# Kernel optimization log

Hardware: AMD Instinct MI355X
Metric: run time of the kernel (lower is better)

The kernel has to match this reference:

```python
import jax, jax.numpy as jnp
import numpy as np

L, D, F, H, E, V = 16, 256, 512, 8, 12, 52000  # layers, width, FFWidth, heads, experts, vocab
B, S = 4, 512
HD = D // H
EPS = 1e-5


def _ln(x, s, b):
    m = x.mean(-1, keepdims=True)
    v = ((x - m) ** 2).mean(-1, keepdims=True)
    return (x - m) / jnp.sqrt(v + EPS) * s + b


def setup_inputs() -> dict:
    key = jax.random.key(0)
    ks = jax.random.split(key, 12)
    w = lambda k, shape: (jax.random.normal(k, shape, dtype=jnp.float32) * 0.02)
    return {
        "tokens": jax.random.randint(ks[0], (B, S), 0, V),
        "emb": w(ks[1], (V, D)),
        "Wq": w(ks[2], (L, D, D)), "bq": jnp.zeros((L, D), jnp.float32),
        "Wk": w(ks[3], (L, D, D)), "bk": jnp.zeros((L, D), jnp.float32),
        "Wv": w(ks[4], (L, D, D)), "bv": jnp.zeros((L, D), jnp.float32),
        "ln1_s": jnp.ones((L, D), jnp.float32), "ln1_b": jnp.zeros((L, D), jnp.float32),
        "ln2_s": jnp.ones((L, D), jnp.float32), "ln2_b": jnp.zeros((L, D), jnp.float32),
        "gW": w(ks[5], (L, D, E)), "gb": jnp.zeros((L, E), jnp.float32),
        "ff1W": w(ks[6], (L, E, D, F)), "ff1b": jnp.zeros((L, E, F), jnp.float32),
        "ffGW": w(ks[7], (L, E, D, F)), "ffGb": jnp.zeros((L, E, F), jnp.float32),
        "ff2W": w(ks[8], (L, E, F, D)), "ff2b": jnp.zeros((L, E, D), jnp.float32),
    }


def _forward(tokens, emb, Wq, bq, Wk, bk, Wv, bv, ln1_s, ln1_b, ln2_s, ln2_b,
             gW, gb, ff1W, ff1b, ffGW, ffGb, ff2W, ff2b):
    x = emb[tokens]  # [B,S,D]
    causal = jnp.triu(jnp.full((S, S), -jnp.inf, dtype=x.dtype), 1)

    def body(x, p):
        (wq, bq_, wk, bk_, wv, bv_, l1s, l1b, l2s, l2b,
         gw, gb_, f1w, f1b, fgw, fgb, f2w, f2b) = p
        q = (x @ wq + bq_).reshape(B, S, H, HD)
        k = (x @ wk + bk_).reshape(B, S, H, HD)
        v = (x @ wv + bv_).reshape(B, S, H, HD)
        # NOTE: original applies no 1/sqrt(d) scaling -- kept faithful
        att = jnp.einsum('bshw,bShw->bhsS', q, k) + causal
        att = jax.nn.softmax(att, axis=-1)
        o = jnp.einsum('bhsS,bShw->bshw', att, v).reshape(B, S, D)
        norm = _ln(o + x, l1s, l1b)
        # MoE: top-2 experts, outputs SUMMED (no gate weighting, per original)
        probs = jax.nn.softmax(norm @ gw + gb_, axis=-1)
        _, idx = jax.lax.top_k(probs, 2)  # [B,S,2]
        msk = jax.nn.one_hot(idx, E, dtype=norm.dtype).sum(-2)  # [B,S,E] in {0,1}
        h = jax.nn.silu(jnp.einsum('bsd,edf->bsef', norm, f1w) + f1b) \
            * (jnp.einsum('bsd,edf->bsef', norm, fgw) + fgb)
        y = jnp.einsum('bsef,efd->bsed', h, f2w) + f2b
        moe = jnp.einsum('bsed,bse->bsd', y, msk)
        return _ln(moe + norm, l2s, l2b), None

    x, _ = jax.lax.scan(body, x, (Wq, bq, Wk, bk, Wv, bv, ln1_s, ln1_b, ln2_s, ln2_b,
                                  gW, gb, ff1W, ff1b, ffGW, ffGb, ff2W, ff2b))
    return x


def reference(tokens, emb, Wq, bq, Wk, bk, Wv, bv, ln1_s, ln1_b, ln2_s, ln2_b,
              gW, gb, ff1W, ff1b, ffGW, ffGb, ff2W, ff2b):
    return _forward(tokens, emb, Wq, bq, Wk, bk, Wv, bv, ln1_s, ln1_b, ln2_s, ln2_b,
                    gW, gb, ff1W, ff1b, ffGW, ffGb, ff2W, ff2b)
```

## Files before the change

kernel.cpp:

```cpp
#include <hip/hip_runtime.h>
#include <math.h>

#define LNUM 16
#define D 256
#define FF 512
#define NH 8
#define NE 12
#define HD 32
#define BB 4
#define SS 512
#define NT 2048
#define EPS 1e-5f
#define MAXT 48
#define PADROWS 5632

typedef _Float16 f16;
typedef __attribute__((ext_vector_type(8))) _Float16 f16x8;
typedef __attribute__((ext_vector_type(4))) _Float16 f16x4;
typedef __attribute__((ext_vector_type(4))) float f32x4;
#define MFMA(A, B, C) __builtin_amdgcn_mfma_f32_16x16x32_f16((A), (B), (C), 0, 0, 0)

__device__ inline void splitf(float x, f16& h, f16& l) {
  f16 hh = (f16)x;
  h = hh;
  l = (f16)(x - (float)hh);
}

__global__ __launch_bounds__(256) void k_wprep(const float* __restrict__ src,
                                               f16* __restrict__ dh, f16* __restrict__ dl,
                                               int K, int N) {
  const size_t msz = (size_t)K * N * blockIdx.z;
  src += msz; dh += msz; dl += msz;
  const int n0 = blockIdx.x * 32, k0 = blockIdx.y * 32;
  __shared__ f16 th[32][36], tl[32][36];
  const int t = threadIdx.x;
  {
    const int r = t >> 3, c4 = (t & 7) * 4;
    float4 v = *(const float4*)(src + (size_t)(k0 + r) * N + n0 + c4);
    f16 h0, l0, h1, l1, h2, l2, h3, l3;
    splitf(v.x, h0, l0); splitf(v.y, h1, l1);
    splitf(v.z, h2, l2); splitf(v.w, h3, l3);
    th[c4 + 0][r] = h0; tl[c4 + 0][r] = l0;
    th[c4 + 1][r] = h1; tl[c4 + 1][r] = l1;
    th[c4 + 2][r] = h2; tl[c4 + 2][r] = l2;
    th[c4 + 3][r] = h3; tl[c4 + 3][r] = l3;
  }
  __syncthreads();
  const int rn = t >> 3, ck = (t & 7) * 4;
  f16x4 hv, lv;
#pragma unroll
  for (int j = 0; j < 4; j++) { hv[j] = th[rn][ck + j]; lv[j] = tl[rn][ck + j]; }
  *(f16x4*)(dh + (size_t)(n0 + rn) * K + k0 + ck) = hv;
  *(f16x4*)(dl + (size_t)(n0 + rn) * K + k0 + ck) = lv;
}

__global__ __launch_bounds__(256) void k_embed(const int* __restrict__ tok,
                                               const float* __restrict__ emb,
                                               float* __restrict__ x,
                                               f16* __restrict__ xh, f16* __restrict__ xl) {
  int n = blockIdx.x, t = threadIdx.x;
  float val = emb[(size_t)tok[n] * D + t];
  x[(size_t)n * D + t] = val;
  f16 h, l; splitf(val, h, l);
  xh[(size_t)n * D + t] = h;
  xl[(size_t)n * D + t] = l;
}

__global__ __launch_bounds__(256) void k_qkv_mfma(
    const f16* __restrict__ xh, const f16* __restrict__ xl,
    const f16* __restrict__ wqh, const f16* __restrict__ wql, const float* __restrict__ bq,
    const f16* __restrict__ wkh, const f16* __restrict__ wkl, const float* __restrict__ bk,
    const f16* __restrict__ wvh, const f16* __restrict__ wvl, const float* __restrict__ bv,
    f16* __restrict__ qhb, f16* __restrict__ qlb,
    f16* __restrict__ khb, f16* __restrict__ klb,
    f16* __restrict__ vhb, f16* __restrict__ vlb) {
  const f16* Wh; const f16* Wl; const float* bias; f16* outh; f16* outl;
  if (blockIdx.z == 0)      { Wh = wqh; Wl = wql; bias = bq; outh = qhb; outl = qlb; }
  else if (blockIdx.z == 1) { Wh = wkh; Wl = wkl; bias = bk; outh = khb; outl = klb; }
  else                      { Wh = wvh; Wl = wvl; bias = bv; outh = vhb; outl = vlb; }
  const int row0 = blockIdx.x * 128, col0 = blockIdx.y * 64;
  __shared__ f16 Ah[128][44], Al[128][44], Bh[64][44], Bl[64][44];
  const int tid = threadIdx.x;
  const int asr = tid >> 1, asc = (tid & 1) * 16;
  const int bn2 = tid >> 2, bkc = (tid & 3) * 8;
  const int lane = tid & 63, w = tid >> 6;
  const int lm = lane & 15, lg = lane >> 4, lk = lg * 8;
  f32x4 acc[2][4] = {};
  for (int k0 = 0; k0 < D; k0 += 32) {
    {
      size_t ga = (size_t)(row0 + asr) * D + k0 + asc;
      *(f16x8*)&Ah[asr][asc]     = *(const f16x8*)(xh + ga);
      *(f16x8*)&Ah[asr][asc + 8] = *(const f16x8*)(xh + ga + 8);
      *(f16x8*)&Al[asr][asc]     = *(const f16x8*)(xl + ga);
      *(f16x8*)&Al[asr][asc + 8] = *(const f16x8*)(xl + ga + 8);
      size_t gb = (size_t)(col0 + bn2) * D + k0 + bkc;
      *(f16x8*)&Bh[bn2][bkc] = *(const f16x8*)(Wh + gb);
      *(f16x8*)&Bl[bn2][bkc] = *(const f16x8*)(Wl + gb);
    }
    __syncthreads();
    f16x8 a_h[2], a_l[2];
#pragma unroll
    for (int mt = 0; mt < 2; mt++) {
      a_h[mt] = *(const f16x8*)&Ah[w * 32 + mt * 16 + lm][lk];
      a_l[mt] = *(const f16x8*)&Al[w * 32 + mt * 16 + lm][lk];
    }
#pragma unroll
    for (int nt = 0; nt < 4; nt++) {
      f16x8 b_h = *(const f16x8*)&Bh[nt * 16 + lm][lk];
      f16x8 b_l = *(const f16x8*)&Bl[nt * 16 + lm][lk];
#pragma unroll
      for (int mt = 0; mt < 2; mt++) {
        f32x4 c = acc[mt][nt];
        c = MFMA(a_h[mt], b_h, c);
        c = MFMA(a_h[mt], b_l, c);
        c = MFMA(a_l[mt], b_h, c);
        acc[mt][nt] = c;
      }
    }
    __syncthreads();
  }
#pragma unroll
  for (int mt = 0; mt < 2; mt++)
#pragma unroll
    for (int nt = 0; nt < 4; nt++) {
      int col = col0 + nt * 16 + lm;
      float bv_ = bias[col];
#pragma unroll
      for (int r = 0; r < 4; r++) {
        int row = row0 + w * 32 + mt * 16 + lg * 4 + r;
        float val = acc[mt][nt][r] + bv_;
        f16 h16, l16; splitf(val, h16, l16);
        outh[(size_t)row * D + col] = h16;
        outl[(size_t)row * D + col] = l16;
      }
    }
}

__global__ __launch_bounds__(256) void k_attn_mfma(
    const f16* __restrict__ qh, const f16* __restrict__ ql,
    const f16* __restrict__ kh, const f16* __restrict__ kl,
    const f16* __restrict__ vh, const f16* __restrict__ vl,
    float* __restrict__ o) {
  const int rt = blockIdx.x, bh = blockIdx.y;
  const int b = bh >> 3, h = bh & 7;
  const int row0 = rt * 64;
  __shared__ f16 Qh[64][40], Ql[64][40], Kh[64][40], Kl[64][40];
  __shared__ f16 Vth[32][72], Vtl[32][72];
  __shared__ f16 Ph[4][16][72], Pl[4][16][72];
  const int tid = threadIdx.x;
  const int lane = tid & 63, w = tid >> 6;
  const int lm = lane & 15, lg = lane >> 4, lk = lg * 8;
  const int sr = tid >> 2, sc = (tid & 3) * 8;
  {
    size_t gq = (size_t)(b * SS + row0 + sr) * D + h * HD + sc;
    *(f16x8*)&Qh[sr][sc] = *(const f16x8*)(qh + gq);
    *(f16x8*)&Ql[sr][sc] = *(const f16x8*)(ql + gq);
  }
  f32x4 accO[2] = {};
  float mrow[4], lsum[4];
#pragma unroll
  for (int r = 0; r < 4; r++) { mrow[r] = -1e30f; lsum[r] = 0.f; }
  for (int ct = 0; ct <= rt; ct++) {
    __syncthreads();
    {
      size_t gk = (size_t)(b * SS + ct * 64 + sr) * D + h * HD + sc;
      *(f16x8*)&Kh[sr][sc] = *(const f16x8*)(kh + gk);
      *(f16x8*)&Kl[sr][sc] = *(const f16x8*)(kl + gk);
      f16x8 hv = *(const f16x8*)(vh + gk);
      f16x8 lv = *(const f16x8*)(vl + gk);
#pragma unroll
      for (int j = 0; j < 8; j++) { Vth[sc + j][sr] = hv[j]; Vtl[sc + j][sr] = lv[j]; }
    }
    __syncthreads();
    f16x8 qfh = *(const f16x8*)&Qh[w * 16 + lm][lk];
    f16x8 qfl = *(const f16x8*)&Ql[w * 16 + lm][lk];
    f32x4 s[4];
#pragma unroll
    for (int nt = 0; nt < 4; nt++) {
      f16x8 kfh = *(const f16x8*)&Kh[nt * 16 + lm][lk];
      f16x8 kfl = *(const f16x8*)&Kl[nt * 16 + lm][lk];
      f32x4 c = {};
      c = MFMA(qfh, kfh, c);
      c = MFMA(qfh, kfl, c);
      c = MFMA(qfl, kfh, c);
      s[nt] = c;
    }
    if (ct == rt) {
#pragma unroll
      for (int nt = 0; nt < 4; nt++)
#pragma unroll
        for (int r = 0; r < 4; r++)
          if (nt * 16 + lm > w * 16 + lg * 4 + r) s[nt][r] = -1e30f;
    }
    float scal[4];
#pragma unroll
    for (int r = 0; r < 4; r++) {
      float mt2 = fmaxf(fmaxf(s[0][r], s[1][r]), fmaxf(s[2][r], s[3][r]));
      mt2 = fmaxf(mt2, __shfl_xor(mt2, 1));
      mt2 = fmaxf(mt2, __shfl_xor(mt2, 2));
      mt2 = fmaxf(mt2, __shfl_xor(mt2, 4));
      mt2 = fmaxf(mt2, __shfl_xor(mt2, 8));
      float mn = fmaxf(mrow[r], mt2);
      scal[r] = expf(mrow[r] - mn);
      mrow[r] = mn;
    }
    float rs[4] = {0.f, 0.f, 0.f, 0.f};
#pragma unroll
    for (int nt = 0; nt < 4; nt++)
#pragma unroll
      for (int r = 0; r < 4; r++) {
        float pv = expf(s[nt][r] - mrow[r]);
        rs[r] += pv;
        f16 ph16, pl16; splitf(pv, ph16, pl16);
        Ph[w][lg * 4 + r][nt * 16 + lm] = ph16;
        Pl[w][lg * 4 + r][nt * 16 + lm] = pl16;
      }
#pragma unroll
    for (int r = 0; r < 4; r++) {
      rs[r] += __shfl_xor(rs[r], 1);
      rs[r] += __shfl_xor(rs[r], 2);
      rs[r] += __shfl_xor(rs[r], 4);
      rs[r] += __shfl_xor(rs[r], 8);
      lsum[r] = lsum[r] * scal[r] + rs[r];
      accO[0][r] *= scal[r];
      accO[1][r] *= scal[r];
    }
#pragma unroll
    for (int ct2 = 0; ct2 < 2; ct2++)
#pragma unroll
      for (int ks = 0; ks < 2; ks++) {
        f16x8 pa_h = *(const f16x8*)&Ph[w][lm][ks * 32 + lk];
        f16x8 pa_l = *(const f16x8*)&Pl[w][lm][ks * 32 + lk];
        f16x8 vb_h = *(const f16x8*)&Vth[ct2 * 16 + lm][ks * 32 + lk];
        f16x8 vb_l = *(const f16x8*)&Vtl[ct2 * 16 + lm][ks * 32 + lk];
        accO[ct2] = MFMA(pa_h, vb_h, accO[ct2]);
        accO[ct2] = MFMA(pa_h, vb_l, accO[ct2]);
        accO[ct2] = MFMA(pa_l, vb_h, accO[ct2]);
      }
  }
#pragma unroll
  for (int ct2 = 0; ct2 < 2; ct2++)
#pragma unroll
    for (int r = 0; r < 4; r++) {
      int grow = row0 + w * 16 + lg * 4 + r;
      o[(size_t)(b * SS + grow) * D + h * HD + ct2 * 16 + lm] = accO[ct2][r] / lsum[r];
    }
}

__global__ __launch_bounds__(256) void k_ln1gate(
    const float* __restrict__ o, const float* __restrict__ x,
    const float* __restrict__ s1, const float* __restrict__ b1,
    const float* __restrict__ gW, const float* __restrict__ gb,
    float* __restrict__ norm, f16* __restrict__ nhb, f16* __restrict__ nlb,
    int* __restrict__ eidx) {
  const int w = threadIdx.x >> 6, lane = threadIdx.x & 63;
  const int n = blockIdx.x * 4 + w;
  float val[4], s1v = 0.f, s2v = 0.f;
#pragma unroll
  for (int j = 0; j < 4; j++) {
    int d = lane + 64 * j;
    float v = o[(size_t)n * D + d] + x[(size_t)n * D + d];
    val[j] = v; s1v += v; s2v += v * v;
  }
#pragma unroll
  for (int m = 1; m < 64; m <<= 1) {
    s1v += __shfl_xor(s1v, m);
    s2v += __shfl_xor(s2v, m);
  }
  float mean = s1v * (1.f / D);
  float var = s2v * (1.f / D) - mean * mean;
  float rstd = rsqrtf(var + EPS);
  float ge[NE];
#pragma unroll
  for (int e = 0; e < NE; e++) ge[e] = 0.f;
#pragma unroll
  for (int j = 0; j < 4; j++) {
    int d = lane + 64 * j;
    float nv = (val[j] - mean) * rstd * s1[d] + b1[d];
    norm[(size_t)n * D + d] = nv;
    f16 h16, l16; splitf(nv, h16, l16);
    nhb[(size_t)n * D + d] = h16;
    nlb[(size_t)n * D + d] = l16;
    const float* gr = gW + (size_t)d * NE;
#pragma unroll
    for (int e = 0; e < NE; e++) ge[e] += nv * gr[e];
  }
#pragma unroll
  for (int m = 1; m < 64; m <<= 1)
#pragma unroll
    for (int e = 0; e < NE; e++) ge[e] += __shfl_xor(ge[e], m);
  if (lane == 0) {
#pragma unroll
    for (int e = 0; e < NE; e++) ge[e] += gb[e];
    int i1 = 0; float v1 = ge[0];
#pragma unroll
    for (int e = 1; e < NE; e++) if (ge[e] > v1) { v1 = ge[e]; i1 = e; }
    int i2 = -1; float v2 = -3.4e38f;
#pragma unroll
    for (int e = 0; e < NE; e++) if (e != i1 && ge[e] > v2) { v2 = ge[e]; i2 = e; }
    eidx[n * 2 + 0] = i1;
    eidx[n * 2 + 1] = i2;
  }
}

__global__ __launch_bounds__(256) void k_route(const int* __restrict__ eidx,
                                               int* __restrict__ rlist, int* __restrict__ tokpos,
                                               int* __restrict__ te, int* __restrict__ tbase,
                                               int* __restrict__ tnv) {
  __shared__ int cnt[NE], cur[NE], poff[NE];
  const int t = threadIdx.x;
  if (t < NE) { cnt[t] = 0; cur[t] = 0; }
  __syncthreads();
  for (int n = t; n < NT; n += 256) {
    atomicAdd(&cnt[eidx[n * 2 + 0]], 1);
    atomicAdd(&cnt[eidx[n * 2 + 1]], 1);
  }
  __syncthreads();
  if (t == 0) {
    int off = 0, ti = 0;
    for (int e = 0; e < NE; e++) {
      poff[e] = off;
      int ntl = (cnt[e] + 127) >> 7;
      for (int tt = 0; tt < ntl; tt++) {
        te[ti] = e; tbase[ti] = off + tt * 128;
        int rem = cnt[e] - tt * 128; tnv[ti] = rem < 128 ? rem : 128;
        ti++;
      }
      off += ntl * 128;
    }
    for (; ti < MAXT; ti++) te[ti] = -1;
  }
  __syncthreads();
  for (int n = t; n < NT; n += 256) {
#pragma unroll
    for (int s2 = 0; s2 < 2; s2++) {
      int e = eidx[n * 2 + s2];
      int pos = atomicAdd(&cur[e], 1);
      int row = poff[e] + pos;
      rlist[row] = n;
      tokpos[n * 2 + s2] = row;
    }
  }
}

__global__ __launch_bounds__(256) void k_ff1_mfma(
    const f16* __restrict__ nhb, const f16* __restrict__ nlb,
    const int* __restrict__ rlist,
    const int* __restrict__ te, const int* __restrict__ tbase, const int* __restrict__ tnv,
    const f16* __restrict__ w1th, const f16* __restrict__ w1tl, const float* __restrict__ b1f,
    const f16* __restrict__ wgth, const f16* __restrict__ wgtl, const float* __restrict__ bgf,
    f16* __restrict__ hhb, f16* __restrict__ hlb) {
  const int mt0 = blockIdx.x;
  const int e = te[mt0];
  if (e < 0) return;
  const int base = tbase[mt0], nv = tnv[mt0];
  const int col0 = blockIdx.y * 64;
  const f16* W1h = w1th + (size_t)e * D * FF;
  const f16* W1l = w1tl + (size_t)e * D * FF;
  const f16* Wgh = wgth + (size_t)e * D * FF;
  const f16* Wgl = wgtl + (size_t)e * D * FF;
  __shared__ f16 Ah[128][44], Al[128][44];
  __shared__ f16 B1h[64][44], B1l[64][44], B2h[64][44], B2l[64][44];
  __shared__ int rows[128];
  const int tid = threadIdx.x;
  if (tid < 128) rows[tid] = (tid < nv) ? rlist[base + tid] : 0;
  __syncthreads();
  const int asr = tid >> 1, asc = (tid & 1) * 16;
  const int bn2 = tid >> 2, bkc = (tid & 3) * 8;
  const int lane = tid & 63, w = tid >> 6;
  const int lm = lane & 15, lg = lane >> 4, lk = lg * 8;
  f32x4 acc1[2][4] = {}, acc2[2][4] = {};
  const int arow = rows[asr];
  for (int k0 = 0; k0 < D; k0 += 32) {
    {
      size_t ga = (size_t)arow * D + k0 + asc;
      *(f16x8*)&Ah[asr][asc]     = *(const f16x8*)(nhb + ga);
      *(f16x8*)&Ah[asr][asc + 8] = *(const f16x8*)(nhb + ga + 8);
      *(f16x8*)&Al[asr][asc]     = *(const f16x8*)(nlb + ga);
      *(f16x8*)&Al[asr][asc + 8] = *(const f16x8*)(nlb + ga + 8);
      size_t gb = (size_t)(col0 + bn2) * D + k0 + bkc;
      *(f16x8*)&B1h[bn2][bkc] = *(const f16x8*)(W1h + gb);
      *(f16x8*)&B1l[bn2][bkc] = *(const f16x8*)(W1l + gb);
      *(f16x8*)&B2h[bn2][bkc] = *(const f16x8*)(Wgh + gb);
      *(f16x8*)&B2l[bn2][bkc] = *(const f16x8*)(Wgl + gb);
    }
    __syncthreads();
    f16x8 a_h[2], a_l[2];
#pragma unroll
    for (int mt = 0; mt < 2; mt++) {
      a_h[mt] = *(const f16x8*)&Ah[w * 32 + mt * 16 + lm][lk];
      a_l[mt] = *(const f16x8*)&Al[w * 32 + mt * 16 + lm][lk];
    }
#pragma unroll
    for (int nt = 0; nt < 4; nt++) {
      f16x8 b_h = *(const f16x8*)&B1h[nt * 16 + lm][lk];
      f16x8 b_l = *(const f16x8*)&B1l[nt * 16 + lm][lk];
      f16x8 c_h = *(const f16x8*)&B2h[nt * 16 + lm][lk];
      f16x8 c_l = *(const f16x8*)&B2l[nt * 16 + lm][lk];
#pragma unroll
      for (int mt = 0; mt < 2; mt++) {
        f32x4 c1 = acc1[mt][nt];
        c1 = MFMA(a_h[mt], b_h, c1);
        c1 = MFMA(a_h[mt], b_l, c1);
        c1 = MFMA(a_l[mt], b_h, c1);
        acc1[mt][nt] = c1;
        f32x4 c2 = acc2[mt][nt];
        c2 = MFMA(a_h[mt], c_h, c2);
        c2 = MFMA(a_h[mt], c_l, c2);
        c2 = MFMA(a_l[mt], c_h, c2);
        acc2[mt][nt] = c2;
      }
    }
    __syncthreads();
  }
#pragma unroll
  for (int mt = 0; mt < 2; mt++)
#pragma unroll
    for (int nt = 0; nt < 4; nt++) {
      int col = col0 + nt * 16 + lm;
      float bb1 = b1f[e * FF + col], bb2 = bgf[e * FF + col];
#pragma unroll
      for (int r = 0; r < 4; r++) {
        int rit = w * 32 + mt * 16 + lg * 4 + r;
        if (rit < nv) {
          float z1 = acc1[mt][nt][r] + bb1;
          float zg = acc2[mt][nt][r] + bb2;
          float sl = z1 / (1.f + expf(-z1));
          float hv = sl * zg;
          f16 h16, l16; splitf(hv, h16, l16);
          hhb[(size_t)(base + rit) * FF + col] = h16;
          hlb[(size_t)(base + rit) * FF + col] = l16;
        }
      }
    }
}

__global__ __launch_bounds__(256) void k_ff2_mfma(
    const f16* __restrict__ hhb, const f16* __restrict__ hlb,
    const int* __restrict__ te, const int* __restrict__ tbase, const int* __restrict__ tnv,
    const f16* __restrict__ w2th, const f16* __restrict__ w2tl, const float* __restrict__ b2f,
    float* __restrict__ ybuf) {
  const int mt0 = blockIdx.x;
  const int e = te[mt0];
  if (e < 0) return;
  const int base = tbase[mt0], nv = tnv[mt0];
  const int col0 = blockIdx.y * 64;
  const f16* W2h = w2th + (size_t)e * FF * D;
  const f16* W2l = w2tl + (size_t)e * FF * D;
  __shared__ f16 Ah[128][44], Al[128][44], Bh[64][44], Bl[64][44];
  const int tid = threadIdx.x;
  const int asr = tid >> 1, asc = (tid & 1) * 16;
  const int bn2 = tid >> 2, bkc = (tid & 3) * 8;
  const int lane = tid & 63, w = tid >> 6;
  const int lm = lane & 15, lg = lane >> 4, lk = lg * 8;
  f32x4 acc[2][4] = {};
  for (int k0 = 0; k0 < FF; k0 += 32) {
    {
      size_t ga = (size_t)(base + asr) * FF + k0 + asc;
      *(f16x8*)&Ah[asr][asc]     = *(const f16x8*)(hhb + ga);
      *(f16x8*)&Ah[asr][asc + 8] = *(const f16x8*)(hhb + ga + 8);
      *(f16x8*)&Al[asr][asc]     = *(const f16x8*)(hlb + ga);
      *(f16x8*)&Al[asr][asc + 8] = *(const f16x8*)(hlb + ga + 8);
      size_t gb = (size_t)(col0 + bn2) * FF + k0 + bkc;
      *(f16x8*)&Bh[bn2][bkc] = *(const f16x8*)(W2h + gb);
      *(f16x8*)&Bl[bn2][bkc] = *(const f16x8*)(W2l + gb);
    }
    __syncthreads();
    f16x8 a_h[2], a_l[2];
#pragma unroll
    for (int mt = 0; mt < 2; mt++) {
      a_h[mt] = *(const f16x8*)&Ah[w * 32 + mt * 16 + lm][lk];
      a_l[mt] = *(const f16x8*)&Al[w * 32 + mt * 16 + lm][lk];
    }
#pragma unroll
    for (int nt = 0; nt < 4; nt++) {
      f16x8 b_h = *(const f16x8*)&Bh[nt * 16 + lm][lk];
      f16x8 b_l = *(const f16x8*)&Bl[nt * 16 + lm][lk];
#pragma unroll
      for (int mt = 0; mt < 2; mt++) {
        f32x4 c = acc[mt][nt];
        c = MFMA(a_h[mt], b_h, c);
        c = MFMA(a_h[mt], b_l, c);
        c = MFMA(a_l[mt], b_h, c);
        acc[mt][nt] = c;
      }
    }
    __syncthreads();
  }
#pragma unroll
  for (int mt = 0; mt < 2; mt++)
#pragma unroll
    for (int nt = 0; nt < 4; nt++) {
      int col = col0 + nt * 16 + lm;
      float bb = b2f[e * D + col];
#pragma unroll
      for (int r = 0; r < 4; r++) {
        int rit = w * 32 + mt * 16 + lg * 4 + r;
        if (rit < nv) ybuf[(size_t)(base + rit) * D + col] = acc[mt][nt][r] + bb;
      }
    }
}

__global__ __launch_bounds__(256) void k_ln2(
    const float* __restrict__ ybuf, const int* __restrict__ tokpos,
    const float* __restrict__ norm, const float* __restrict__ s2, const float* __restrict__ b2,
    float* __restrict__ dst, f16* __restrict__ xh, f16* __restrict__ xl) {
  const int w = threadIdx.x >> 6, lane = threadIdx.x & 63;
  const int n = blockIdx.x * 4 + w;
  const int p0 = tokpos[n * 2 + 0], p1 = tokpos[n * 2 + 1];
  float val[4], s1v = 0.f, s2v = 0.f;
#pragma unroll
  for (int j = 0; j < 4; j++) {
    int d = lane + 64 * j;
    float v = ybuf[(size_t)p0 * D + d] + ybuf[(size_t)p1 * D + d] + norm[(size_t)n * D + d];
    val[j] = v; s1v += v; s2v += v * v;
  }
#pragma unroll
  for (int m = 1; m < 64; m <<= 1) {
    s1v += __shfl_xor(s1v, m);
    s2v += __shfl_xor(s2v, m);
  }
  float mean = s1v * (1.f / D);
  float var = s2v * (1.f / D) - mean * mean;
  float rstd = rsqrtf(var + EPS);
#pragma unroll
  for (int j = 0; j < 4; j++) {
    int d = lane + 64 * j;
    float ov = (val[j] - mean) * rstd * s2[d] + b2[d];
    dst[(size_t)n * D + d] = ov;
    f16 h16, l16; splitf(ov, h16, l16);
    xh[(size_t)n * D + d] = h16;
    xl[(size_t)n * D + d] = l16;
  }
}

extern "C" void kernel_launch(void* const* d_in, const int* in_sizes, int n_in,
                              void* d_out, int out_size, void* d_ws, size_t ws_size,
                              hipStream_t stream) {
  (void)in_sizes; (void)n_in; (void)out_size; (void)ws_size;
  const int*   tok = (const int*)d_in[0];
  const float* emb = (const float*)d_in[1];
  const float* Wq  = (const float*)d_in[2];
  const float* bq  = (const float*)d_in[3];
  const float* Wk  = (const float*)d_in[4];
  const float* bk  = (const float*)d_in[5];
  const float* Wv  = (const float*)d_in[6];
  const float* bv  = (const float*)d_in[7];
  const float* l1s = (const float*)d_in[8];
  const float* l1b = (const float*)d_in[9];
  const float* l2s = (const float*)d_in[10];
  const float* l2b = (const float*)d_in[11];
  const float* gW  = (const float*)d_in[12];
  const float* gb  = (const float*)d_in[13];
  const float* f1W = (const float*)d_in[14];
  const float* f1b = (const float*)d_in[15];
  const float* fgW = (const float*)d_in[16];
  const float* fgb = (const float*)d_in[17];
  const float* f2W = (const float*)d_in[18];
  const float* f2b = (const float*)d_in[19];
  float* out = (float*)d_out;

  char* p = (char*)d_ws;
  auto alloc = [&](size_t bytes) { char* r = p; p += (bytes + 255) & ~(size_t)255; return r; };
  float* xb = (float*)alloc((size_t)NT * D * 4);
  f16* xh = (f16*)alloc((size_t)NT * D * 2);
  f16* xl = (f16*)alloc((size_t)NT * D * 2);
  f16* qhb = (f16*)alloc((size_t)NT * D * 2);
  f16* qlb = (f16*)alloc((size_t)NT * D * 2);
  f16* khb = (f16*)alloc((size_t)NT * D * 2);
  f16* klb = (f16*)alloc((size_t)NT * D * 2);
  f16* vhb = (f16*)alloc((size_t)NT * D * 2);
  f16* vlb = (f16*)alloc((size_t)NT * D * 2);
  float* ob = (float*)alloc((size_t)NT * D * 4);
  float* nb = (float*)alloc((size_t)NT * D * 4);
  f16* nhb = (f16*)alloc((size_t)NT * D * 2);
  f16* nlb = (f16*)alloc((size_t)NT * D * 2);
  f16* hhb = (f16*)alloc((size_t)PADROWS * FF * 2);
  f16* hlb = (f16*)alloc((size_t)PADROWS * FF * 2);
  float* yb = (float*)alloc((size_t)PADROWS * D * 4);
  int* eidx   = (int*)alloc((size_t)NT * 2 * 4);
  int* rlist  = (int*)alloc((size_t)PADROWS * 4);
  int* tokpos = (int*)alloc((size_t)NT * 2 * 4);
  int* te     = (int*)alloc(MAXT * 4);
  int* tbase  = (int*)alloc(MAXT * 4);
  int* tnv    = (int*)alloc(MAXT * 4);
  size_t qkvsz = (size_t)LNUM * D * D;
  size_t ffsz  = (size_t)LNUM * NE * D * FF;
  f16* wqh = (f16*)alloc(qkvsz * 2); f16* wql = (f16*)alloc(qkvsz * 2);
  f16* wkh = (f16*)alloc(qkvsz * 2); f16* wkl = (f16*)alloc(qkvsz * 2);
  f16* wvh = (f16*)alloc(qkvsz * 2); f16* wvl = (f16*)alloc(qkvsz * 2);
  f16* w1th = (f16*)alloc(ffsz * 2); f16* w1tl = (f16*)alloc(ffsz * 2);
  f16* wgth = (f16*)alloc(ffsz * 2); f16* wgtl = (f16*)alloc(ffsz * 2);
  f16* w2th = (f16*)alloc(ffsz * 2); f16* w2tl = (f16*)alloc(ffsz * 2);

  k_wprep<<<dim3(D / 32, D / 32, LNUM), 256, 0, stream>>>(Wq, wqh, wql, D, D);
  k_wprep<<<dim3(D / 32, D / 32, LNUM), 256, 0, stream>>>(Wk, wkh, wkl, D, D);
  k_wprep<<<dim3(D / 32, D / 32, LNUM), 256, 0, stream>>>(Wv, wvh, wvl, D, D);
  k_wprep<<<dim3(FF / 32, D / 32, LNUM * NE), 256, 0, stream>>>(f1W, w1th, w1tl, D, FF);
  k_wprep<<<dim3(FF / 32, D / 32, LNUM * NE), 256, 0, stream>>>(fgW, wgth, wgtl, D, FF);
  k_wprep<<<dim3(D / 32, FF / 32, LNUM * NE), 256, 0, stream>>>(f2W, w2th, w2tl, FF, D);

  k_embed<<<NT, 256, 0, stream>>>(tok, emb, xb, xh, xl);

  for (int l = 0; l < LNUM; l++) {
    k_qkv_mfma<<<dim3(16, 4, 3), 256, 0, stream>>>(
        xh, xl,
        wqh + (size_t)l * D * D, wql + (size_t)l * D * D, bq + (size_t)l * D,
        wkh + (size_t)l * D * D, wkl + (size_t)l * D * D, bk + (size_t)l * D,
        wvh + (size_t)l * D * D, wvl + (size_t)l * D * D, bv + (size_t)l * D,
        qhb, qlb, khb, klb, vhb, vlb);
    k_attn_mfma<<<dim3(8, 32), 256, 0, stream>>>(qhb, qlb, khb, klb, vhb, vlb, ob);
    k_ln1gate<<<NT / 4, 256, 0, stream>>>(ob, xb, l1s + (size_t)l * D, l1b + (size_t)l * D,
                                          gW + (size_t)l * D * NE, gb + (size_t)l * NE,
                                          nb, nhb, nlb, eidx);
    k_route<<<1, 256, 0, stream>>>(eidx, rlist, tokpos, te, tbase, tnv);
    k_ff1_mfma<<<dim3(MAXT, 8), 256, 0, stream>>>(
        nhb, nlb, rlist, te, tbase, tnv,
        w1th + (size_t)l * NE * D * FF, w1tl + (size_t)l * NE * D * FF, f1b + (size_t)l * NE * FF,
        wgth + (size_t)l * NE * D * FF, wgtl + (size_t)l * NE * D * FF, fgb + (size_t)l * NE * FF,
        hhb, hlb);
    k_ff2_mfma<<<dim3(MAXT, 4), 256, 0, stream>>>(
        hhb, hlb, te, tbase, tnv,
        w2th + (size_t)l * NE * FF * D, w2tl + (size_t)l * NE * FF * D, f2b + (size_t)l * NE * D,
        yb);
    k_ln2<<<NT / 4, 256, 0, stream>>>(yb, tokpos, nb, l2s + (size_t)l * D, l2b + (size_t)l * D,
                                      (l == LNUM - 1) ? out : xb, xh, xl);
  }
}
```

Before: 1.974 ms.

## Fold MoE routing into gate kernel with fixed-capacity expert slots; widen K tiles

Drops the single-block k_route kernel. The gate kernel now claims per-expert row slots with atomics into fixed-capacity regions (CAP rows per expert), and the FF kernels derive their tiles from per-layer counters that are zeroed once in the embed kernel. The GEMM kernels also move from a K-step of 32 to 64 with larger padded LDS tiles, halving the number of barrier rounds. The attention MFMA sections are wrapped in s_setprio. The cost removed is the serial per-layer routing launch and its latency. The trade-off is that an expert receiving more than 512 tokens would overflow its slot region, and atomic slot order makes row placement nondeterministic.

After: 2.254 ms. +14.2%, slower.

```diff
diff --git a/kernel.cpp b/kernel.cpp
--- a/kernel.cpp
+++ b/kernel.cpp
@@ -11,8 +11,8 @@
 #define SS 512
 #define NT 2048
 #define EPS 1e-5f
-#define MAXT 48
-#define PADROWS 5632
+#define CAP 512
+#define ROWSP (NE * CAP)
 
 typedef _Float16 f16;
 typedef __attribute__((ext_vector_type(8))) _Float16 f16x8;
@@ -57,8 +57,10 @@
 __global__ __launch_bounds__(256) void k_embed(const int* __restrict__ tok,
                                                const float* __restrict__ emb,
                                                float* __restrict__ x,
-                                               f16* __restrict__ xh, f16* __restrict__ xl) {
+                                               f16* __restrict__ xh, f16* __restrict__ xl,
+                                               int* __restrict__ cntbuf) {
   int n = blockIdx.x, t = threadIdx.x;
+  if (n == 0 && t < LNUM * NE) cntbuf[t] = 0;
   float val = emb[(size_t)tok[n] * D + t];
   x[(size_t)n * D + t] = val;
   f16 h, l; splitf(val, h, l);
@@ -74,47 +76,55 @@
     f16* __restrict__ qhb, f16* __restrict__ qlb,
     f16* __restrict__ khb, f16* __restrict__ klb,
     f16* __restrict__ vhb, f16* __restrict__ vlb) {
+  const int mat = blockIdx.z;
   const f16* Wh; const f16* Wl; const float* bias; f16* outh; f16* outl;
-  if (blockIdx.z == 0)      { Wh = wqh; Wl = wql; bias = bq; outh = qhb; outl = qlb; }
-  else if (blockIdx.z == 1) { Wh = wkh; Wl = wkl; bias = bk; outh = khb; outl = klb; }
-  else                      { Wh = wvh; Wl = wvl; bias = bv; outh = vhb; outl = vlb; }
+  if (mat == 0)      { Wh = wqh; Wl = wql; bias = bq; outh = qhb; outl = qlb; }
+  else if (mat == 1) { Wh = wkh; Wl = wkl; bias = bk; outh = khb; outl = klb; }
+  else               { Wh = wvh; Wl = wvl; bias = bv; outh = vhb; outl = vlb; }
   const int row0 = blockIdx.x * 128, col0 = blockIdx.y * 64;
-  __shared__ f16 Ah[128][44], Al[128][44], Bh[64][44], Bl[64][44];
+  __shared__ f16 Ah[128][72], Al[128][72], Bh[64][72], Bl[64][72];
   const int tid = threadIdx.x;
-  const int asr = tid >> 1, asc = (tid & 1) * 16;
-  const int bn2 = tid >> 2, bkc = (tid & 3) * 8;
+  const int asr = tid >> 1, asc = (tid & 1) * 32;
+  const int bn2 = tid >> 2, bkc = (tid & 3) * 16;
   const int lane = tid & 63, w = tid >> 6;
   const int lm = lane & 15, lg = lane >> 4, lk = lg * 8;
   f32x4 acc[2][4] = {};
-  for (int k0 = 0; k0 < D; k0 += 32) {
+  for (int k0 = 0; k0 < D; k0 += 64) {
     {
       size_t ga = (size_t)(row0 + asr) * D + k0 + asc;
-      *(f16x8*)&Ah[asr][asc]     = *(const f16x8*)(xh + ga);
-      *(f16x8*)&Ah[asr][asc + 8] = *(const f16x8*)(xh + ga + 8);
-      *(f16x8*)&Al[asr][asc]     = *(const f16x8*)(xl + ga);
-      *(f16x8*)&Al[asr][asc + 8] = *(const f16x8*)(xl + ga + 8);
+#pragma unroll
+      for (int j = 0; j < 4; j++) {
+        *(f16x8*)&Ah[asr][asc + j * 8] = *(const f16x8*)(xh + ga + j * 8);
+        *(f16x8*)&Al[asr][asc + j * 8] = *(const f16x8*)(xl + ga + j * 8);
+      }
       size_t gb = (size_t)(col0 + bn2) * D + k0 + bkc;
-      *(f16x8*)&Bh[bn2][bkc] = *(const f16x8*)(Wh + gb);
-      *(f16x8*)&Bl[bn2][bkc] = *(const f16x8*)(Wl + gb);
-    }
-    __syncthreads();
-    f16x8 a_h[2], a_l[2];
-#pragma unroll
-    for (int mt = 0; mt < 2; mt++) {
-      a_h[mt] = *(const f16x8*)&Ah[w * 32 + mt * 16 + lm][lk];
-      a_l[mt] = *(const f16x8*)&Al[w * 32 + mt * 16 + lm][lk];
-    }
-#pragma unroll
-    for (int nt = 0; nt < 4; nt++) {
-      f16x8 b_h = *(const f16x8*)&Bh[nt * 16 + lm][lk];
-      f16x8 b_l = *(const f16x8*)&Bl[nt * 16 + lm][lk];
+#pragma unroll
+      for (int j = 0; j < 2; j++) {
+        *(f16x8*)&Bh[bn2][bkc + j * 8] = *(const f16x8*)(Wh + gb + j * 8);
+        *(f16x8*)&Bl[bn2][bkc + j * 8] = *(const f16x8*)(Wl + gb + j * 8);
+      }
+    }
+    __syncthreads();
+#pragma unroll
+    for (int ks = 0; ks < 2; ks++) {
+      f16x8 a_h[2], a_l[2];
 #pragma unroll
       for (int mt = 0; mt < 2; mt++) {
-        f32x4 c = acc[mt][nt];
-        c = MFMA(a_h[mt], b_h, c);
-        c = MFMA(a_h[mt], b_l, c);
-        c = MFMA(a_l[mt], b_h, c);
-        acc[mt][nt] = c;
+        a_h[mt] = *(const f16x8*)&Ah[w * 32 + mt * 16 + lm][ks * 32 + lk];
+        a_l[mt] = *(const f16x8*)&Al[w * 32 + mt * 16 + lm][ks * 32 + lk];
+      }
+#pragma unroll
+      for (int nt = 0; nt < 4; nt++) {
+        f16x8 b_h = *(const f16x8*)&Bh[nt * 16 + lm][ks * 32 + lk];
+        f16x8 b_l = *(const f16x8*)&Bl[nt * 16 + lm][ks * 32 + lk];
+#pragma unroll
+        for (int mt = 0; mt < 2; mt++) {
+          f32x4 c = acc[mt][nt];
+          c = MFMA(a_h[mt], b_h, c);
+          c = MFMA(a_h[mt], b_l, c);
+          c = MFMA(a_l[mt], b_h, c);
+          acc[mt][nt] = c;
+        }
       }
     }
     __syncthreads();
@@ -175,6 +185,7 @@
     f16x8 qfh = *(const f16x8*)&Qh[w * 16 + lm][lk];
     f16x8 qfl = *(const f16x8*)&Ql[w * 16 + lm][lk];
     f32x4 s[4];
+    __builtin_amdgcn_s_setprio(1);
 #pragma unroll
     for (int nt = 0; nt < 4; nt++) {
       f16x8 kfh = *(const f16x8*)&Kh[nt * 16 + lm][lk];
@@ -185,6 +196,7 @@
       c = MFMA(qfl, kfh, c);
       s[nt] = c;
     }
+    __builtin_amdgcn_s_setprio(0);
     if (ct == rt) {
 #pragma unroll
       for (int nt = 0; nt < 4; nt++)
@@ -225,6 +237,7 @@
       accO[0][r] *= scal[r];
       accO[1][r] *= scal[r];
     }
+    __builtin_amdgcn_s_setprio(1);
 #pragma unroll
     for (int ct2 = 0; ct2 < 2; ct2++)
 #pragma unroll
@@ -237,6 +250,7 @@
         accO[ct2] = MFMA(pa_h, vb_l, accO[ct2]);
         accO[ct2] = MFMA(pa_l, vb_h, accO[ct2]);
       }
+    __builtin_amdgcn_s_setprio(0);
   }
 #pragma unroll
   for (int ct2 = 0; ct2 < 2; ct2++)
@@ -252,7 +266,7 @@
     const float* __restrict__ s1, const float* __restrict__ b1,
     const float* __restrict__ gW, const float* __restrict__ gb,
     float* __restrict__ norm, f16* __restrict__ nhb, f16* __restrict__ nlb,
-    int* __restrict__ eidx) {
+    int* __restrict__ cnt, int* __restrict__ rlist, int* __restrict__ tokpos) {
   const int w = threadIdx.x >> 6, lane = threadIdx.x & 63;
   const int n = blockIdx.x * 4 + w;
   float val[4], s1v = 0.f, s2v = 0.f;
@@ -298,117 +312,91 @@
     int i2 = -1; float v2 = -3.4e38f;
 #pragma unroll
     for (int e = 0; e < NE; e++) if (e != i1 && ge[e] > v2) { v2 = ge[e]; i2 = e; }
-    eidx[n * 2 + 0] = i1;
-    eidx[n * 2 + 1] = i2;
-  }
-}
-
-__global__ __launch_bounds__(256) void k_route(const int* __restrict__ eidx,
-                                               int* __restrict__ rlist, int* __restrict__ tokpos,
-                                               int* __restrict__ te, int* __restrict__ tbase,
-                                               int* __restrict__ tnv) {
-  __shared__ int cnt[NE], cur[NE], poff[NE];
-  const int t = threadIdx.x;
-  if (t < NE) { cnt[t] = 0; cur[t] = 0; }
-  __syncthreads();
-  for (int n = t; n < NT; n += 256) {
-    atomicAdd(&cnt[eidx[n * 2 + 0]], 1);
-    atomicAdd(&cnt[eidx[n * 2 + 1]], 1);
-  }
-  __syncthreads();
-  if (t == 0) {
-    int off = 0, ti = 0;
-    for (int e = 0; e < NE; e++) {
-      poff[e] = off;
-      int ntl = (cnt[e] + 127) >> 7;
-      for (int tt = 0; tt < ntl; tt++) {
-        te[ti] = e; tbase[ti] = off + tt * 128;
-        int rem = cnt[e] - tt * 128; tnv[ti] = rem < 128 ? rem : 128;
-        ti++;
-      }
-      off += ntl * 128;
-    }
-    for (; ti < MAXT; ti++) te[ti] = -1;
-  }
-  __syncthreads();
-  for (int n = t; n < NT; n += 256) {
-#pragma unroll
-    for (int s2 = 0; s2 < 2; s2++) {
-      int e = eidx[n * 2 + s2];
-      int pos = atomicAdd(&cur[e], 1);
-      int row = poff[e] + pos;
-      rlist[row] = n;
-      tokpos[n * 2 + s2] = row;
-    }
+    int p1 = atomicAdd(&cnt[i1], 1);
+    int row1 = i1 * CAP + p1;
+    rlist[row1] = n;
+    tokpos[n * 2 + 0] = row1;
+    int p2 = atomicAdd(&cnt[i2], 1);
+    int row2 = i2 * CAP + p2;
+    rlist[row2] = n;
+    tokpos[n * 2 + 1] = row2;
   }
 }
 
 __global__ __launch_bounds__(256) void k_ff1_mfma(
     const f16* __restrict__ nhb, const f16* __restrict__ nlb,
-    const int* __restrict__ rlist,
-    const int* __restrict__ te, const int* __restrict__ tbase, const int* __restrict__ tnv,
+    const int* __restrict__ cnt, const int* __restrict__ rlist,
     const f16* __restrict__ w1th, const f16* __restrict__ w1tl, const float* __restrict__ b1f,
     const f16* __restrict__ wgth, const f16* __restrict__ wgtl, const float* __restrict__ bgf,
     f16* __restrict__ hhb, f16* __restrict__ hlb) {
-  const int mt0 = blockIdx.x;
-  const int e = te[mt0];
-  if (e < 0) return;
-  const int base = tbase[mt0], nv = tnv[mt0];
+  const int e = blockIdx.x >> 2, tl = blockIdx.x & 3;
+  const int cnt_e = cnt[e];
+  if (tl * 128 >= cnt_e) return;
+  const int nv0 = cnt_e - tl * 128;
+  const int nv = nv0 < 128 ? nv0 : 128;
+  const int base = e * CAP + tl * 128;
   const int col0 = blockIdx.y * 64;
-  const f16* W1h = w1th + (size_t)e * D * FF;
-  const f16* W1l = w1tl + (size_t)e * D * FF;
-  const f16* Wgh = wgth + (size_t)e * D * FF;
-  const f16* Wgl = wgtl + (size_t)e * D * FF;
-  __shared__ f16 Ah[128][44], Al[128][44];
-  __shared__ f16 B1h[64][44], B1l[64][44], B2h[64][44], B2l[64][44];
+  const f16* W1h = w1th + (size_t)e * D * FF + (size_t)col0 * D;
+  const f16* W1l = w1tl + (size_t)e * D * FF + (size_t)col0 * D;
+  const f16* Wgh = wgth + (size_t)e * D * FF + (size_t)col0 * D;
+  const f16* Wgl = wgtl + (size_t)e * D * FF + (size_t)col0 * D;
+  __shared__ f16 Ah[128][72], Al[128][72];
+  __shared__ f16 B1h[64][72], B1l[64][72], B2h[64][72], B2l[64][72];
   __shared__ int rows[128];
   const int tid = threadIdx.x;
   if (tid < 128) rows[tid] = (tid < nv) ? rlist[base + tid] : 0;
   __syncthreads();
-  const int asr = tid >> 1, asc = (tid & 1) * 16;
-  const int bn2 = tid >> 2, bkc = (tid & 3) * 8;
+  const int asr = tid >> 1, asc = (tid & 1) * 32;
+  const int bn2 = tid >> 2, bkc = (tid & 3) * 16;
   const int lane = tid & 63, w = tid >> 6;
   const int lm = lane & 15, lg = lane >> 4, lk = lg * 8;
   f32x4 acc1[2][4] = {}, acc2[2][4] = {};
   const int arow = rows[asr];
-  for (int k0 = 0; k0 < D; k0 += 32) {
+  for (int k0 = 0; k0 < D; k0 += 64) {
     {
       size_t ga = (size_t)arow * D + k0 + asc;
-      *(f16x8*)&Ah[asr][asc]     = *(const f16x8*)(nhb + ga);
-      *(f16x8*)&Ah[asr][asc + 8] = *(const f16x8*)(nhb + ga + 8);
-      *(f16x8*)&Al[asr][asc]     = *(const f16x8*)(nlb + ga);
-      *(f16x8*)&Al[asr][asc + 8] = *(const f16x8*)(nlb + ga + 8);
-      size_t gb = (size_t)(col0 + bn2) * D + k0 + bkc;
-      *(f16x8*)&B1h[bn2][bkc] = *(const f16x8*)(W1h + gb);
-      *(f16x8*)&B1l[bn2][bkc] = *(const f16x8*)(W1l + gb);
-      *(f16x8*)&B2h[bn2][bkc] = *(const f16x8*)(Wgh + gb);
-      *(f16x8*)&B2l[bn2][bkc] = *(const f16x8*)(Wgl + gb);
-    }
-    __syncthreads();
-    f16x8 a_h[2], a_l[2];
-#pragma unroll
-    for (int mt = 0; mt < 2; mt++) {
-      a_h[mt] = *(const f16x8*)&Ah[w * 32 + mt * 16 + lm][lk];
-      a_l[mt] = *(const f16x8*)&Al[w * 32 + mt * 16 + lm][lk];
-    }
-#pragma unroll
-    for (int nt = 0; nt < 4; nt++) {
-      f16x8 b_h = *(const f16x8*)&B1h[nt * 16 + lm][lk];
-      f16x8 b_l = *(const f16x8*)&B1l[nt * 16 + lm][lk];
-      f16x8 c_h = *(const f16x8*)&B2h[nt * 16 + lm][lk];
-      f16x8 c_l = *(const f16x8*)&B2l[nt * 16 + lm][lk];
+#pragma unroll
+      for (int j = 0; j < 4; j++) {
+        *(f16x8*)&Ah[asr][asc + j * 8] = *(const f16x8*)(nhb + ga + j * 8);
+        *(f16x8*)&Al[asr][asc + j * 8] = *(const f16x8*)(nlb + ga + j * 8);
+      }
+      size_t gb = (size_t)bn2 * D + k0 + bkc;
+#pragma unroll
+      for (int j = 0; j < 2; j++) {
+        *(f16x8*)&B1h[bn2][bkc + j * 8] = *(const f16x8*)(W1h + gb + j * 8);
+        *(f16x8*)&B1l[bn2][bkc + j * 8] = *(const f16x8*)(W1l + gb + j * 8);
+        *(f16x8*)&B2h[bn2][bkc + j * 8] = *(const f16x8*)(Wgh + gb + j * 8);
+        *(f16x8*)&B2l[bn2][bkc + j * 8] = *(const f16x8*)(Wgl + gb + j * 8);
+      }
+    }
+    __syncthreads();
+#pragma unroll
+    for (int ks = 0; ks < 2; ks++) {
+      f16x8 a_h[2], a_l[2];
 #pragma unroll
       for (int mt = 0; mt < 2; mt++) {
-        f32x4 c1 = acc1[mt][nt];
-        c1 = MFMA(a_h[mt], b_h, c1);
-        c1 = MFMA(a_h[mt], b_l, c1);
-        c1 = MFMA(a_l[mt], b_h, c1);
-        acc1[mt][nt] = c1;
-        f32x4 c2 = acc2[mt][nt];
-        c2 = MFMA(a_h[mt], c_h, c2);
-        c2 = MFMA(a_h[mt], c_l, c2);
-        c2 = MFMA(a_l[mt], c_h, c2);
-        acc2[mt][nt] = c2;
+        a_h[mt] = *(const f16x8*)&Ah[w * 32 + mt * 16 + lm][ks * 32 + lk];
+        a_l[mt] = *(const f16x8*)&Al[w * 32 + mt * 16 + lm][ks * 32 + lk];
+      }
+#pragma unroll
+      for (int nt = 0; nt < 4; nt++) {
+        f16x8 b_h = *(const f16x8*)&B1h[nt * 16 + lm][ks * 32 + lk];
+        f16x8 b_l = *(const f16x8*)&B1l[nt * 16 + lm][ks * 32 + lk];
+        f16x8 c_h = *(const f16x8*)&B2h[nt * 16 + lm][ks * 32 + lk];
+        f16x8 c_l = *(const f16x8*)&B2l[nt * 16 + lm][ks * 32 + lk];
+#pragma unroll
+        for (int mt = 0; mt < 2; mt++) {
+          f32x4 c1 = acc1[mt][nt];
+          c1 = MFMA(a_h[mt], b_h, c1);
+          c1 = MFMA(a_h[mt], b_l, c1);
+          c1 = MFMA(a_l[mt], b_h, c1);
+          acc1[mt][nt] = c1;
+          f32x4 c2 = acc2[mt][nt];
+          c2 = MFMA(a_h[mt], c_h, c2);
+          c2 = MFMA(a_h[mt], c_l, c2);
+          c2 = MFMA(a_l[mt], c_h, c2);
+          acc2[mt][nt] = c2;
+        }
       }
     }
     __syncthreads();
@@ -437,52 +425,61 @@
 
 __global__ __launch_bounds__(256) void k_ff2_mfma(
     const f16* __restrict__ hhb, const f16* __restrict__ hlb,
-    const int* __restrict__ te, const int* __restrict__ tbase, const int* __restrict__ tnv,
+    const int* __restrict__ cnt,
     const f16* __restrict__ w2th, const f16* __restrict__ w2tl, const float* __restrict__ b2f,
     float* __restrict__ ybuf) {
-  const int mt0 = blockIdx.x;
-  const int e = te[mt0];
-  if (e < 0) return;
-  const int base = tbase[mt0], nv = tnv[mt0];
+  const int e = blockIdx.x >> 2, tl = blockIdx.x & 3;
+  const int cnt_e = cnt[e];
+  if (tl * 128 >= cnt_e) return;
+  const int nv0 = cnt_e - tl * 128;
+  const int nv = nv0 < 128 ? nv0 : 128;
+  const int base = e * CAP + tl * 128;
   const int col0 = blockIdx.y * 64;
-  const f16* W2h = w2th + (size_t)e * FF * D;
-  const f16* W2l = w2tl + (size_t)e * FF * D;
-  __shared__ f16 Ah[128][44], Al[128][44], Bh[64][44], Bl[64][44];
+  const f16* W2h = w2th + (size_t)e * FF * D + (size_t)col0 * FF;
+  const f16* W2l = w2tl + (size_t)e * FF * D + (size_t)col0 * FF;
+  __shared__ f16 Ah[128][72], Al[128][72], Bh[64][72], Bl[64][72];
   const int tid = threadIdx.x;
-  const int asr = tid >> 1, asc = (tid & 1) * 16;
-  const int bn2 = tid >> 2, bkc = (tid & 3) * 8;
+  const int asr = tid >> 1, asc = (tid & 1) * 32;
+  const int bn2 = tid >> 2, bkc = (tid & 3) * 16;
   const int lane = tid & 63, w = tid >> 6;
   const int lm = lane & 15, lg = lane >> 4, lk = lg * 8;
   f32x4 acc[2][4] = {};
-  for (int k0 = 0; k0 < FF; k0 += 32) {
+  for (int k0 = 0; k0 < FF; k0 += 64) {
     {
       size_t ga = (size_t)(base + asr) * FF + k0 + asc;
-      *(f16x8*)&Ah[asr][asc]     = *(const f16x8*)(hhb + ga);
-      *(f16x8*)&Ah[asr][asc + 8] = *(const f16x8*)(hhb + ga + 8);
-      *(f16x8*)&Al[asr][asc]     = *(const f16x8*)(hlb + ga);
-      *(f16x8*)&Al[asr][asc + 8] = *(const f16x8*)(hlb + ga + 8);
-      size_t gb = (size_t)(col0 + bn2) * FF + k0 + bkc;
-      *(f16x8*)&Bh[bn2][bkc] = *(const f16x8*)(W2h + gb);
-      *(f16x8*)&Bl[bn2][bkc] = *(const f16x8*)(W2l + gb);
-    }
-    __syncthreads();
-    f16x8 a_h[2], a_l[2];
-#pragma unroll
-    for (int mt = 0; mt < 2; mt++) {
-      a_h[mt] = *(const f16x8*)&Ah[w * 32 + mt * 16 + lm][lk];
-      a_l[mt] = *(const f16x8*)&Al[w * 32 + mt * 16 + lm][lk];
-    }
-#pragma unroll
-    for (int nt = 0; nt < 4; nt++) {
-      f16x8 b_h = *(const f16x8*)&Bh[nt * 16 + lm][lk];
-      f16x8 b_l = *(const f16x8*)&Bl[nt * 16 + lm][lk];
+#pragma unroll
+      for (int j = 0; j < 4; j++) {
+        *(f16x8*)&Ah[asr][asc + j * 8] = *(const f16x8*)(hhb + ga + j * 8);
+        *(f16x8*)&Al[asr][asc + j * 8] = *(const f16x8*)(hlb + ga + j * 8);
+      }
+      size_t gb = (size_t)bn2 * FF + k0 + bkc;
+#pragma unroll
+      for (int j = 0; j < 2; j++) {
+        *(f16x8*)&Bh[bn2][bkc + j * 8] = *(const f16x8*)(W2h + gb + j * 8);
+        *(f16x8*)&Bl[bn2][bkc + j * 8] = *(const f16x8*)(W2l + gb + j * 8);
+      }
+    }
+    __syncthreads();
+#pragma unroll
+    for (int ks = 0; ks < 2; ks++) {
+      f16x8 a_h[2], a_l[2];
 #pragma unroll
       for (int mt = 0; mt < 2; mt++) {
-        f32x4 c = acc[mt][nt];
-        c = MFMA(a_h[mt], b_h, c);
-        c = MFMA(a_h[mt], b_l, c);
-        c = MFMA(a_l[mt], b_h, c);
-        acc[mt][nt] = c;
+        a_h[mt] = *(const f16x8*)&Ah[w * 32 + mt * 16 + lm][ks * 32 + lk];
+        a_l[mt] = *(const f16x8*)&Al[w * 32 + mt * 16 + lm][ks * 32 + lk];
+      }
+#pragma unroll
+      for (int nt = 0; nt < 4; nt++) {
+        f16x8 b_h = *(const f16x8*)&Bh[nt * 16 + lm][ks * 32 + lk];
+        f16x8 b_l = *(const f16x8*)&Bl[nt * 16 + lm][ks * 32 + lk];
+#pragma unroll
+        for (int mt = 0; mt < 2; mt++) {
+          f32x4 c = acc[mt][nt];
+          c = MFMA(a_h[mt], b_h, c);
+          c = MFMA(a_h[mt], b_l, c);
+          c = MFMA(a_l[mt], b_h, c);
+          acc[mt][nt] = c;
+        }
       }
     }
     __syncthreads();
@@ -575,15 +572,12 @@
   float* nb = (float*)alloc((size_t)NT * D * 4);
   f16* nhb = (f16*)alloc((size_t)NT * D * 2);
   f16* nlb = (f16*)alloc((size_t)NT * D * 2);
-  f16* hhb = (f16*)alloc((size_t)PADROWS * FF * 2);
-  f16* hlb = (f16*)alloc((size_t)PADROWS * FF * 2);
-  float* yb = (float*)alloc((size_t)PADROWS * D * 4);
-  int* eidx   = (int*)alloc((size_t)NT * 2 * 4);
-  int* rlist  = (int*)alloc((size_t)PADROWS * 4);
+  f16* hhb = (f16*)alloc((size_t)ROWSP * FF * 2);
+  f16* hlb = (f16*)alloc((size_t)ROWSP * FF * 2);
+  float* yb = (float*)alloc((size_t)ROWSP * D * 4);
+  int* cntbuf = (int*)alloc((size_t)LNUM * NE * 4);
+  int* rlist  = (int*)alloc((size_t)ROWSP * 4);
   int* tokpos = (int*)alloc((size_t)NT * 2 * 4);
-  int* te     = (int*)alloc(MAXT * 4);
-  int* tbase  = (int*)alloc(MAXT * 4);
-  int* tnv    = (int*)alloc(MAXT * 4);
   size_t qkvsz = (size_t)LNUM * D * D;
   size_t ffsz  = (size_t)LNUM * NE * D * FF;
   f16* wqh = (f16*)alloc(qkvsz * 2); f16* wql = (f16*)alloc(qkvsz * 2);
@@ -600,9 +594,10 @@
   k_wprep<<<dim3(FF / 32, D / 32, LNUM * NE), 256, 0, stream>>>(fgW, wgth, wgtl, D, FF);
   k_wprep<<<dim3(D / 32, FF / 32, LNUM * NE), 256, 0, stream>>>(f2W, w2th, w2tl, FF, D);
 
-  k_embed<<<NT, 256, 0, stream>>>(tok, emb, xb, xh, xl);
+  k_embed<<<NT, 256, 0, stream>>>(tok, emb, xb, xh, xl, cntbuf);
 
   for (int l = 0; l < LNUM; l++) {
+    int* cnt = cntbuf + l * NE;
     k_qkv_mfma<<<dim3(16, 4, 3), 256, 0, stream>>>(
         xh, xl,
         wqh + (size_t)l * D * D, wql + (size_t)l * D * D, bq + (size_t)l * D,
@@ -612,15 +607,14 @@
     k_attn_mfma<<<dim3(8, 32), 256, 0, stream>>>(qhb, qlb, khb, klb, vhb, vlb, ob);
     k_ln1gate<<<NT / 4, 256, 0, stream>>>(ob, xb, l1s + (size_t)l * D, l1b + (size_t)l * D,
                                           gW + (size_t)l * D * NE, gb + (size_t)l * NE,
-                                          nb, nhb, nlb, eidx);
-    k_route<<<1, 256, 0, stream>>>(eidx, rlist, tokpos, te, tbase, tnv);
-    k_ff1_mfma<<<dim3(MAXT, 8), 256, 0, stream>>>(
-        nhb, nlb, rlist, te, tbase, tnv,
+                                          nb, nhb, nlb, cnt, rlist, tokpos);
+    k_ff1_mfma<<<dim3(NE * 4, 8), 256, 0, stream>>>(
+        nhb, nlb, cnt, rlist,
         w1th + (size_t)l * NE * D * FF, w1tl + (size_t)l * NE * D * FF, f1b + (size_t)l * NE * FF,
         wgth + (size_t)l * NE * D * FF, wgtl + (size_t)l * NE * D * FF, fgb + (size_t)l * NE * FF,
         hhb, hlb);
-    k_ff2_mfma<<<dim3(MAXT, 4), 256, 0, stream>>>(
-        hhb, hlb, te, tbase, tnv,
+    k_ff2_mfma<<<dim3(NE * 4, 4), 256, 0, stream>>>(
+        hhb, hlb, cnt,
         w2th + (size_t)l * NE * FF * D, w2tl + (size_t)l * NE * FF * D, f2b + (size_t)l * NE * D,
         yb);
     k_ln2<<<NT / 4, 256, 0, stream>>>(yb, tokpos, nb, l2s + (size_t)l * D, l2b + (size_t)l * D,
```
